# Kernel optimization log

Hardware: AMD Instinct MI355X
Metric: run time of the kernel (lower is better)

The kernel has to match this reference:

```python
import jax, jax.numpy as jnp
import numpy as np
import math

FACTOR = 5

def setup_inputs() -> dict:
    key = jax.random.key(0)
    k1, k2, k3, k4 = jax.random.split(key, 4)
    B, L, H, D = 4, 4096, 8, 64
    sample_k = min(FACTOR * int(np.ceil(np.log(L))), L)  # 45
    return {
        "queries": jax.random.normal(k1, (B, L, H, D), dtype=jnp.float32),
        "keys": jax.random.normal(k2, (B, L, H, D), dtype=jnp.float32),
        "values": jax.random.normal(k3, (B, L, H, D), dtype=jnp.float32),
        "index_sample": jax.random.randint(k4, (L, sample_k), 0, L, dtype=jnp.int64),
    }

def reference(queries, keys, values, index_sample):
    # [B, L, H, D] -> [B, H, L, D]
    Q = jnp.transpose(queries, (0, 2, 1, 3))
    K = jnp.transpose(keys, (0, 2, 1, 3))
    V = jnp.transpose(values, (0, 2, 1, 3))
    b, h, l_q, d = Q.shape
    l_k = K.shape[2]

    # n_top (u) per Informer: factor * ceil(ln(l_q)), capped at l_q
    u = min(FACTOR * int(math.ceil(math.log(l_q))), l_q)

    # --- _prob_QK: sampled QK scores ---
    # K_sample: [b, h, l_q, sample_k, d] via shared per-query random sample
    K_sample = K[:, :, index_sample, :]
    # Q_K_sample: [b, h, l_q, sample_k]
    Q_K_sample = jnp.einsum("bhqd,bhqsd->bhqs", Q, K_sample)
    # sparsity measure M: max - mean(sum/l_k)
    M = Q_K_sample.max(axis=-1) - Q_K_sample.sum(axis=-1) / l_k
    # top-u queries (indices; order irrelevant to the math)
    _, M_top = jax.lax.top_k(M, u)  # [b, h, u]

    # Q_reduce: [b, h, u, d]
    Q_reduce = jnp.take_along_axis(Q, M_top[..., None], axis=2)
    # full scores for selected queries: [b, h, u, l_k]
    scale = 1.0 / math.sqrt(d)
    scores_top = jnp.einsum("bhud,bhkd->bhuk", Q_reduce, K) * scale

    # --- initial context: mean of V broadcast over queries ---
    context = jnp.broadcast_to(V.mean(axis=2, keepdims=True), (b, h, l_q, d))

    # --- update context at selected query positions ---
    attn = jax.nn.softmax(scores_top, axis=-1)          # [b, h, u, l_k]
    upd = jnp.einsum("bhuk,bhkd->bhud", attn, V)         # [b, h, u, d]
    bi = jnp.arange(b)[:, None, None]
    hi = jnp.arange(h)[None, :, None]
    context = context.at[bi, hi, M_top].set(upd)

    # [B, H, L, D] -> [B, L, H, D]
    return jnp.transpose(context, (0, 2, 1, 3))
```

## Files before the change

kernel.cpp:

```cpp
#include <hip/hip_runtime.h>
#include <stdint.h>

#define B_ 4
#define L_ 4096
#define H_ 8
#define D_ 64
#define S_ 45
#define U_ 45
#define BH_ 32
#define KC_ 16
#define STRIDE_ (H_*D_)
#define BSTR_ ((size_t)L_*H_*D_)

__device__ __forceinline__ bool detect_idx64(const int* idxp){
    bool z = true;
    #pragma unroll
    for (int i = 1; i < 32; i += 2) z = z && (idxp[i] == 0);
    return z;
}

__global__ __launch_bounds__(256) void kM(const float* __restrict__ Qb,
                                          const float* __restrict__ Kb,
                                          const int* __restrict__ idxp,
                                          float* __restrict__ Mout){
    int g = blockIdx.x;
    int grp8 = g & 7;
    int b  = grp8 >> 1;
    int hg = grp8 & 1;
    int chunk = g >> 3;
    int q0 = chunk * 16;
    bool idx64 = detect_idx64(idxp);

    __shared__ int lidx[16*S_];
    for (int i = threadIdx.x; i < 16*S_; i += 256)
        lidx[i] = idx64 ? idxp[2*(q0*S_ + i)] : idxp[q0*S_ + i];
    __syncthreads();

    int lane = threadIdx.x & 63;
    int w    = threadIdx.x >> 6;
    int grp  = lane >> 4;
    int l16  = lane & 15;
    int ql   = w*4 + grp;
    int q    = q0 + ql;

    const float4* qr = (const float4*)(Qb + (size_t)b*BSTR_ + (size_t)q*STRIDE_ + hg*256);
    float4 qf0 = qr[l16];
    float4 qf1 = qr[16 + l16];
    float4 qf2 = qr[32 + l16];
    float4 qf3 = qr[48 + l16];

    const float* kbase = Kb + (size_t)b*BSTR_ + hg*256;
    float mxa = -1e30f, mxb = -1e30f, sma = 0.f, smb = 0.f;
    const int* myIdx = &lidx[ql*S_];

    #pragma unroll 3
    for (int s = 0; s < S_; s++){
        int ki = myIdx[s];
        const float4* kr = (const float4*)(kbase + (size_t)ki*STRIDE_);
        float4 k0 = kr[l16], k1 = kr[16+l16], k2 = kr[32+l16], k3 = kr[48+l16];
        float p0 = qf0.x*k0.x; p0 = fmaf(qf0.y,k0.y,p0); p0 = fmaf(qf0.z,k0.z,p0); p0 = fmaf(qf0.w,k0.w,p0);
        float p1 = qf1.x*k1.x; p1 = fmaf(qf1.y,k1.y,p1); p1 = fmaf(qf1.z,k1.z,p1); p1 = fmaf(qf1.w,k1.w,p1);
        float p2 = qf2.x*k2.x; p2 = fmaf(qf2.y,k2.y,p2); p2 = fmaf(qf2.z,k2.z,p2); p2 = fmaf(qf2.w,k2.w,p2);
        float p3 = qf3.x*k3.x; p3 = fmaf(qf3.y,k3.y,p3); p3 = fmaf(qf3.z,k3.z,p3); p3 = fmaf(qf3.w,k3.w,p3);
        float u0 = p0 + __shfl_xor(p0, 8);
        float u1 = p1 + __shfl_xor(p1, 8);
        float u2 = p2 + __shfl_xor(p2, 8);
        float u3 = p3 + __shfl_xor(p3, 8);
        float va = (l16 < 8) ? u0 : u2;
        float vb = (l16 < 8) ? u1 : u3;
        #pragma unroll
        for (int off = 1; off < 8; off <<= 1){
            va += __shfl_xor(va, off);
            vb += __shfl_xor(vb, off);
        }
        mxa = fmaxf(mxa, va); sma += va;
        mxb = fmaxf(mxb, vb); smb += vb;
    }
    int hsel = (l16==0) ? 0 : (l16==1) ? 1 : (l16==8) ? 2 : (l16==9) ? 3 : -1;
    if (hsel >= 0){
        float mv = (l16 & 1) ? mxb : mxa;
        float sv = (l16 & 1) ? smb : sma;
        Mout[(size_t)(b*8 + hg*4 + hsel)*L_ + q] = mv - sv*(1.0f/L_);
    }
}

__global__ __launch_bounds__(512) void kTopF(const float* __restrict__ M,
                                             int* __restrict__ Mtop,
                                             float* __restrict__ meanZ,
                                             int* __restrict__ selRow){
    int bh = blockIdx.x;
    int t = threadIdx.x;
    if (t < 64) meanZ[bh*64 + t] = 0.f;
    for (int j = t; j < L_; j += 512) selRow[(size_t)bh*L_ + j] = 0;

    __shared__ float cV[8*U_];
    __shared__ int   cI[8*U_];
    int wv = t >> 6, lane = t & 63;
    const float* Mr = M + (size_t)bh*L_ + wv*512;
    float v[8];
    #pragma unroll
    for (int j = 0; j < 8; j++) v[j] = Mr[lane + 64*j];

    for (int it = 0; it < U_; it++){
        float best = -1e30f; int bidx = 0x7fffffff;
        #pragma unroll
        for (int j = 0; j < 8; j++){
            int id = lane + 64*j;
            if (v[j] > best){ best = v[j]; bidx = id; }
        }
        #pragma unroll
        for (int off = 1; off < 64; off <<= 1){
            float ov = __shfl_xor(best, off); int oi = __shfl_xor(bidx, off);
            if (ov > best || (ov == best && oi < bidx)){ best = ov; bidx = oi; }
        }
        if (lane == 0){ cV[wv*U_ + it] = best; cI[wv*U_ + it] = wv*512 + bidx; }
        if (lane == (bidx & 63)) v[bidx >> 6] = -1e30f;
    }
    __syncthreads();
    if (t < 64){
        float v2[6]; int id2[6];
        #pragma unroll
        for (int j = 0; j < 6; j++){
            int slot = t + 64*j;
            if (slot < 8*U_){ v2[j] = cV[slot]; id2[j] = cI[slot]; }
            else            { v2[j] = -1e30f;  id2[j] = 0x7fffffff; }
        }
        for (int it = 0; it < U_; it++){
            float best = -1e30f; int bidx = 0x7fffffff; int bj = 0;
            #pragma unroll
            for (int j = 0; j < 6; j++){
                if (v2[j] > best || (v2[j] == best && id2[j] < bidx)){
                    best = v2[j]; bidx = id2[j]; bj = j;
                }
            }
            float myBest = best; int myIdx = bidx;
            #pragma unroll
            for (int off = 1; off < 64; off <<= 1){
                float ov = __shfl_xor(best, off); int oi = __shfl_xor(bidx, off);
                if (ov > best || (ov == best && oi < bidx)){ best = ov; bidx = oi; }
            }
            if (t == 0){
                Mtop[bh*U_ + it] = bidx;
                selRow[(size_t)bh*L_ + bidx] = it + 1;
            }
            if (myBest == best && myIdx == bidx) v2[bj] = -1e30f;
        }
    }
}

__global__ __launch_bounds__(256) void kAttnPart(const float* __restrict__ Qb,
                                                 const float* __restrict__ Kb,
                                                 const float* __restrict__ Vb,
                                                 const int*   __restrict__ Mtop,
                                                 float* __restrict__ Opart,
                                                 float* __restrict__ mlG,
                                                 float* __restrict__ mean){
    int bh = blockIdx.y, b = bh >> 3, h = bh & 7;
    int kc = blockIdx.x, uh = blockIdx.z;
    int u0 = uh ? 23 : 0;
    int nu = uh ? 22 : 23;
    int t = threadIdx.x;
    __shared__ float S[24][260];
    __shared__ float red[4][8][64];
    __shared__ int   qidx[23];

    if (t < nu) qidx[t] = Mtop[bh*U_ + u0 + t];
    __syncthreads();

    int k = kc*256 + t;
    float4 kf[16];
    const float4* K4 = (const float4*)(Kb + (size_t)b*BSTR_ + (size_t)k*STRIDE_ + h*D_);
    #pragma unroll
    for (int c = 0; c < 16; c++) kf[c] = K4[c];
    for (int u = 0; u < nu; u++){
        int qi = __builtin_amdgcn_readfirstlane(qidx[u]);
        const float4* qp = (const float4*)(Qb + (size_t)b*BSTR_ + (size_t)qi*STRIDE_ + h*D_);
        float a0=0.f, a1=0.f, a2=0.f, a3=0.f;
        #pragma unroll
        for (int c = 0; c < 16; c++){
            float4 qv = qp[c];
            a0 = fmaf(qv.x, kf[c].x, a0);
            a1 = fmaf(qv.y, kf[c].y, a1);
            a2 = fmaf(qv.z, kf[c].z, a2);
            a3 = fmaf(qv.w, kf[c].w, a3);
        }
        S[u][t] = ((a0+a1)+(a2+a3)) * 0.125f;
    }
    __syncthreads();

    int wv = t >> 6, lane = t & 63;
    for (int u = wv; u < nu; u += 4){
        float4 sv = *(const float4*)&S[u][lane*4];
        float m = fmaxf(fmaxf(sv.x, sv.y), fmaxf(sv.z, sv.w));
        #pragma unroll
        for (int off = 1; off < 64; off <<= 1) m = fmaxf(m, __shfl_xor(m, off));
        float e0 = __expf(sv.x - m), e1 = __expf(sv.y - m);
        float e2 = __expf(sv.z - m), e3 = __expf(sv.w - m);
        float ls = (e0+e1)+(e2+e3);
        #pragma unroll
        for (int off = 1; off < 64; off <<= 1) ls += __shfl_xor(ls, off);
        float4 pv; pv.x = e0; pv.y = e1; pv.z = e2; pv.w = e3;
        *(float4*)&S[u][lane*4] = pv;
        if (lane == 0){
            size_t mi = ((size_t)(bh*KC_ + kc)*U_ + u0 + u)*2;
            mlG[mi] = m; mlG[mi+1] = ls;
        }
    }
    __syncthreads();

    int d8 = t & 7, ks = t >> 3;
    float vsum[8];
    #pragma unroll
    for (int j = 0; j < 8; j++) vsum[j] = 0.f;
    for (int g = 0; g < 3; g++){
        int g0 = g*8; int nug = (nu - g0 < 8) ? (nu - g0) : 8;
        float acc[8][8];
        #pragma unroll
        for (int r = 0; r < 8; r++)
            #pragma unroll
            for (int j = 0; j < 8; j++) acc[r][j] = 0.f;
        for (int i = 0; i < 8; i++){
            int kk = ks + 32*i;
            const float4* V4 = (const float4*)(Vb + (size_t)b*BSTR_ +
                        (size_t)(kc*256 + kk)*STRIDE_ + h*D_);
            float4 va = V4[d8*2], vb = V4[d8*2+1];
            float vf[8] = {va.x, va.y, va.z, va.w, vb.x, vb.y, vb.z, vb.w};
            if (uh == 0 && g == 0){
                #pragma unroll
                for (int j = 0; j < 8; j++) vsum[j] += vf[j];
            }
            #pragma unroll
            for (int r = 0; r < 8; r++){
                float p = S[g0+r][kk];
                #pragma unroll
                for (int j = 0; j < 8; j++) acc[r][j] = fmaf(p, vf[j], acc[r][j]);
            }
        }
        #pragma unroll
        for (int off = 8; off <= 32; off <<= 1)
            #pragma unroll
            for (int r = 0; r < 8; r++)
                #pragma unroll
                for (int j = 0; j < 8; j++) acc[r][j] += __shfl_xor(acc[r][j], off);
        if (lane < 8){
            for (int r = 0; r < 8; r++)
                #pragma unroll
                for (int j = 0; j < 8; j++) red[wv][r][d8*8+j] = acc[r][j];
        }
        __syncthreads();
        for (int tt = t; tt < nug*64; tt += 256){
            int r = tt >> 6, d = tt & 63;
            float s = red[0][r][d] + red[1][r][d] + red[2][r][d] + red[3][r][d];
            Opart[((size_t)(bh*KC_ + kc)*U_ + u0 + g0 + r)*64 + d] = s;
        }
        __syncthreads();
    }
    if (uh == 0){
        #pragma unroll
        for (int off = 8; off <= 32; off <<= 1)
            #pragma unroll
            for (int j = 0; j < 8; j++) vsum[j] += __shfl_xor(vsum[j], off);
        if (lane < 8){
            #pragma unroll
            for (int j = 0; j < 8; j++) red[wv][0][lane*8 + j] = vsum[j];
        }
        __syncthreads();
        if (t < 64){
            float s = red[0][0][t] + red[1][0][t] + red[2][0][t] + red[3][0][t];
            atomicAdd(&mean[bh*64 + t], s);
        }
    }
}

__global__ __launch_bounds__(256) void kOut(const float* __restrict__ mean,
                                            const int*   __restrict__ selRow,
                                            const float* __restrict__ mlG,
                                            const float* __restrict__ Opart,
                                            float* __restrict__ out){
    size_t t = (size_t)blockIdx.x*256 + threadIdx.x;
    int d16 = (int)(t & 15); int h = (int)((t >> 4) & 7);
    int l   = (int)((t >> 7) & 4095); int b = (int)(t >> 19);
    int bh = b*8 + h;
    int sel = selRow[(size_t)bh*L_ + l];
    float4 o;
    if (sel == 0){
        o = *(const float4*)(mean + bh*64 + d16*4);
        const float inv = 1.0f / L_;
        o.x *= inv; o.y *= inv; o.z *= inv; o.w *= inv;
    } else {
        int u = sel - 1;
        float mstar = -1e30f;
        #pragma unroll
        for (int kc = 0; kc < KC_; kc++)
            mstar = fmaxf(mstar, mlG[((size_t)(bh*KC_ + kc)*U_ + u)*2]);
        float lsum = 0.f;
        float4 acc; acc.x = acc.y = acc.z = acc.w = 0.f;
        #pragma unroll
        for (int kc = 0; kc < KC_; kc++){
            size_t mi = ((size_t)(bh*KC_ + kc)*U_ + u)*2;
            float w = __expf(mlG[mi] - mstar);
            lsum = fmaf(mlG[mi+1], w, lsum);
            float4 op = *(const float4*)(Opart + ((size_t)(bh*KC_ + kc)*U_ + u)*64 + d16*4);
            acc.x = fmaf(w, op.x, acc.x);
            acc.y = fmaf(w, op.y, acc.y);
            acc.z = fmaf(w, op.z, acc.z);
            acc.w = fmaf(w, op.w, acc.w);
        }
        float inv = 1.0f / lsum;
        acc.x *= inv; acc.y *= inv; acc.z *= inv; acc.w *= inv;
        o = acc;
    }
    ((float4*)out)[t] = o;
}

extern "C" void kernel_launch(void* const* d_in, const int* in_sizes, int n_in,
                              void* d_out, int out_size, void* d_ws, size_t ws_size,
                              hipStream_t stream) {
    const float* Qb  = (const float*)d_in[0];
    const float* Kb  = (const float*)d_in[1];
    const float* Vb  = (const float*)d_in[2];
    const int*   idx = (const int*)d_in[3];
    float* out = (float*)d_out;

    float* ws = (float*)d_ws;
    float* M      = ws;
    int*   Mtop   = (int*)(ws + 131072);
    float* mean   = ws + 133120;
    int*   selRow = (int*)(ws + 135168);
    float* mlG    = ws + 266240;
    float* Opart  = ws + 315392;

    kM        <<<dim3(2048),       dim3(256), 0, stream>>>(Qb, Kb, idx, M);
    kTopF     <<<dim3(32),         dim3(512), 0, stream>>>(M, Mtop, mean, selRow);
    kAttnPart <<<dim3(KC_, 32, 2), dim3(256), 0, stream>>>(Qb, Kb, Vb, Mtop, Opart, mlG, mean);
    kOut      <<<dim3(8192),       dim3(256), 0, stream>>>(mean, selRow, mlG, Opart, out);
}
```

Baseline: 333.7 us.

## Restructure P·V partial product so each wave owns query rows and lanes own dims

Replaces the P·V stage, where threads split keys and head dims and then reduced across lanes and waves through shared memory, with a layout where each wave handles 6 selected queries and each lane one output dim, looping over all 256 keys. This removes the cross-lane shuffle reductions, the shared reduction buffer, and several block barriers. Each V element is now read by all four waves, and unused score rows are zero-filled so the fixed 6-row loop needs no bounds checks. The V mean is accumulated by a single wave.

```diff
diff --git a/kernel.cpp b/kernel.cpp
--- a/kernel.cpp
+++ b/kernel.cpp
@@ -161,10 +161,10 @@
     int nu = uh ? 22 : 23;
     int t = threadIdx.x;
     __shared__ float S[24][260];
-    __shared__ float red[4][8][64];
     __shared__ int   qidx[23];
 
     if (t < nu) qidx[t] = Mtop[bh*U_ + u0 + t];
+    for (int i = t; i < (24 - nu)*260; i += 256) (&S[nu][0])[i] = 0.f;
     __syncthreads();
 
     int k = kc*256 + t;
@@ -208,68 +208,33 @@
     }
     __syncthreads();
 
-    int d8 = t & 7, ks = t >> 3;
-    float vsum[8];
+    int d = lane, w = wv;
+    int ub = w*6;
+    int nuw = nu - ub; if (nuw > 6) nuw = 6; if (nuw < 0) nuw = 0;
+    float acc[6];
     #pragma unroll
-    for (int j = 0; j < 8; j++) vsum[j] = 0.f;
-    for (int g = 0; g < 3; g++){
-        int g0 = g*8; int nug = (nu - g0 < 8) ? (nu - g0) : 8;
-        float acc[8][8];
-        #pragma unroll
-        for (int r = 0; r < 8; r++)
-            #pragma unroll
-            for (int j = 0; j < 8; j++) acc[r][j] = 0.f;
-        for (int i = 0; i < 8; i++){
-            int kk = ks + 32*i;
-            const float4* V4 = (const float4*)(Vb + (size_t)b*BSTR_ +
-                        (size_t)(kc*256 + kk)*STRIDE_ + h*D_);
-            float4 va = V4[d8*2], vb = V4[d8*2+1];
-            float vf[8] = {va.x, va.y, va.z, va.w, vb.x, vb.y, vb.z, vb.w};
-            if (uh == 0 && g == 0){
-                #pragma unroll
-                for (int j = 0; j < 8; j++) vsum[j] += vf[j];
-            }
-            #pragma unroll
-            for (int r = 0; r < 8; r++){
-                float p = S[g0+r][kk];
-                #pragma unroll
-                for (int j = 0; j < 8; j++) acc[r][j] = fmaf(p, vf[j], acc[r][j]);
-            }
-        }
-        #pragma unroll
-        for (int off = 8; off <= 32; off <<= 1)
-            #pragma unroll
-            for (int r = 0; r < 8; r++)
-                #pragma unroll
-                for (int j = 0; j < 8; j++) acc[r][j] += __shfl_xor(acc[r][j], off);
-        if (lane < 8){
-            for (int r = 0; r < 8; r++)
-                #pragma unroll
-                for (int j = 0; j < 8; j++) red[wv][r][d8*8+j] = acc[r][j];
-        }
-        __syncthreads();
-        for (int tt = t; tt < nug*64; tt += 256){
-            int r = tt >> 6, d = tt & 63;
-            float s = red[0][r][d] + red[1][r][d] + red[2][r][d] + red[3][r][d];
-            Opart[((size_t)(bh*KC_ + kc)*U_ + u0 + g0 + r)*64 + d] = s;
-        }
-        __syncthreads();
-    }
-    if (uh == 0){
-        #pragma unroll
-        for (int off = 8; off <= 32; off <<= 1)
-            #pragma unroll
-            for (int j = 0; j < 8; j++) vsum[j] += __shfl_xor(vsum[j], off);
-        if (lane < 8){
-            #pragma unroll
-            for (int j = 0; j < 8; j++) red[wv][0][lane*8 + j] = vsum[j];
-        }
-        __syncthreads();
-        if (t < 64){
-            float s = red[0][0][t] + red[1][0][t] + red[2][0][t] + red[3][0][t];
-            atomicAdd(&mean[bh*64 + t], s);
-        }
-    }
+    for (int j = 0; j < 6; j++) acc[j] = 0.f;
+    float vsum = 0.f;
+    const float* Vbase = Vb + (size_t)b*BSTR_ + (size_t)(kc*256)*STRIDE_ + h*D_ + d;
+    for (int kb = 0; kb < 64; kb++){
+        float v0 = Vbase[(size_t)(kb*4+0)*STRIDE_];
+        float v1 = Vbase[(size_t)(kb*4+1)*STRIDE_];
+        float v2 = Vbase[(size_t)(kb*4+2)*STRIDE_];
+        float v3 = Vbase[(size_t)(kb*4+3)*STRIDE_];
+        if (uh == 0 && w == 0) vsum += (v0+v1)+(v2+v3);
+        #pragma unroll
+        for (int j = 0; j < 6; j++){
+            float4 p = *(const float4*)&S[ub+j][kb*4];
+            acc[j] = fmaf(p.x, v0, acc[j]);
+            acc[j] = fmaf(p.y, v1, acc[j]);
+            acc[j] = fmaf(p.z, v2, acc[j]);
+            acc[j] = fmaf(p.w, v3, acc[j]);
+        }
+    }
+    for (int j = 0; j < nuw; j++)
+        Opart[((size_t)(bh*KC_ + kc)*U_ + u0 + ub + j)*64 + d] = acc[j];
+    if (uh == 0 && w == 0)
+        atomicAdd(&mean[bh*64 + d], vsum);
 }
 
 __global__ __launch_bounds__(256) void kOut(const float* __restrict__ mean,
```

Result: faster. 305.9 us (-8.3%).
